# Kernel tuning notes

Hardware: AMD Instinct MI355X
Metric: run time of the kernel (lower is better)

The kernel has to match this reference:

```python
import jax, jax.numpy as jnp
import numpy as np

NB_HEAD = 8
SIZE_PER_HEAD = 64
MAX_LEN = 1024
MASK_PENALTY = 1e12


def setup_inputs() -> dict:
    key = jax.random.key(0)
    ks = jax.random.split(key, 6)
    B, L, D_IN = 8, MAX_LEN, 512
    D_OUT = NB_HEAD * SIZE_PER_HEAD
    return {
        "Q_seq": jax.random.normal(ks[0], (B, L, D_IN), dtype=jnp.float32),
        "K_seq": jax.random.normal(ks[1], (B, L, D_IN), dtype=jnp.float32),
        "V_seq": jax.random.normal(ks[2], (B, L, D_IN), dtype=jnp.float32),
        "WQ": jax.random.normal(ks[3], (D_IN, D_OUT), dtype=jnp.float32) * 0.03,
        "WK": jax.random.normal(ks[4], (D_IN, D_OUT), dtype=jnp.float32) * 0.03,
        "WV": jax.random.normal(ks[5], (D_IN, D_OUT), dtype=jnp.float32) * 0.03,
    }


def reference(Q_seq, K_seq, V_seq, WQ, WK, WV):
    B, L, _ = Q_seq.shape
    H, D = NB_HEAD, SIZE_PER_HEAD
    # project and split heads: [B, L, H*D] -> [B, H, L, D]
    q = (Q_seq @ WQ).reshape(B, L, H, D).transpose(0, 2, 1, 3)
    k = (K_seq @ WK).reshape(B, L, H, D).transpose(0, 2, 1, 3)
    v = (V_seq @ WV).reshape(B, L, H, D).transpose(0, 2, 1, 3)
    scale = 1.0 / jnp.sqrt(jnp.asarray(D, dtype=q.dtype))
    scores = jnp.einsum('bhqd,bhkd->bhqk', q, k) * scale  # [B,H,L,L]
    # Mask(): eye+cumsum construction == causal mask (penalize key > query)
    causal = jnp.triu(jnp.ones((L, L), dtype=scores.dtype), k=1)
    scores = scores - causal * MASK_PENALTY
    A = jax.nn.softmax(scores, axis=-1)
    O = jnp.einsum('bhqk,bhkd->bhqd', A, v)  # [B,H,L,D]
    return O.transpose(0, 2, 1, 3).reshape(B, L, H * D)
```

## Files before the change

kernel.cpp:

```cpp
#include <hip/hip_runtime.h>

#define NH 8
#define DH 64
#define SL 1024
#define NB 8
#define DIN 512
#define DOUT 512
#define PS 72

typedef __bf16 bf16x8 __attribute__((ext_vector_type(8)));
typedef float floatx4 __attribute__((ext_vector_type(4)));
typedef unsigned short ushortx8 __attribute__((ext_vector_type(8)));

__device__ __forceinline__ unsigned short f2bf(float f) {
    unsigned int u = __builtin_bit_cast(unsigned int, f);
    u += 0x7FFFu + ((u >> 16) & 1u);
    return (unsigned short)(u >> 16);
}

__device__ __forceinline__ floatx4 mfma_bf16(bf16x8 a, bf16x8 b, floatx4 c) {
    return __builtin_amdgcn_mfma_f32_16x16x32_bf16(a, b, c, 0, 0, 0);
}

__device__ __forceinline__ void gld_lds16(const unsigned short* g, unsigned short* l) {
    __builtin_amdgcn_global_load_lds(
        (const __attribute__((address_space(1))) unsigned int*)g,
        (__attribute__((address_space(3))) unsigned int*)l, 16, 0, 0);
}

__device__ __forceinline__ unsigned int pack_bf2(float a, float b) {
    return __builtin_amdgcn_perm(__builtin_bit_cast(unsigned int, b),
                                 __builtin_bit_cast(unsigned int, a), 0x07060302u);
}

__global__ __launch_bounds__(256) void xbf_kernel(const float* __restrict__ Qs,
                                                  const float* __restrict__ Ks,
                                                  const float* __restrict__ Vs,
                                                  unsigned short* __restrict__ xb) {
    const int z = blockIdx.y;
    const float* X = (z == 0) ? Qs : (z == 1 ? Ks : Vs);
    const int t = blockIdx.x * 256 + threadIdx.x;
    const int row = t >> 6, c = t & 63;
    const float4 a = *(const float4*)(X + t * 8);
    const float4 b = *(const float4*)(X + t * 8 + 4);
    ushortx8 o;
    o[0] = f2bf(a.x); o[1] = f2bf(a.y); o[2] = f2bf(a.z); o[3] = f2bf(a.w);
    o[4] = f2bf(b.x); o[5] = f2bf(b.y); o[6] = f2bf(b.z); o[7] = f2bf(b.w);
    const int dst = (((row >> 7) * 8 + (c >> 3)) * 128 + (row & 127)) * 64 +
                    (((c & 7) ^ (row & 7)) * 8);
    *(ushortx8*)(xb + z * 8192 * DIN + dst) = o;
}

__global__ __launch_bounds__(256) void wt_kernel(const float* __restrict__ WQ,
                                                 const float* __restrict__ WK,
                                                 const float* __restrict__ WV,
                                                 unsigned short* __restrict__ wt) {
    __shared__ unsigned short tile[64][68];
    const int z = blockIdx.z;
    const float* W = (z == 0) ? WQ : (z == 1 ? WK : WV);
    const int k0 = blockIdx.y * 64, n0 = blockIdx.x * 64;
    const int tn = threadIdx.x & 63, tk = threadIdx.x >> 6;
#pragma unroll
    for (int i = 0; i < 16; ++i) {
        const int kk = tk + i * 4;
        tile[tn][kk] = f2bf(W[(k0 + kk) * DOUT + n0 + tn]);
    }
    __syncthreads();
#pragma unroll
    for (int i = 0; i < 16; ++i) {
        const int nn = tk + i * 4;
        const int n = n0 + nn, k = k0 + tn;
        const int dst = (((z * 4 + (n >> 7)) * 8 + (k >> 6)) * 128 + (n & 127)) * 64 +
                        ((((k >> 3) & 7) ^ (n & 7)) * 8) + (k & 7);
        wt[dst] = tile[nn][tn];
    }
}

__global__ __launch_bounds__(256) void proj_kernel(const unsigned short* __restrict__ xbt,
                                                   const unsigned short* __restrict__ wtt,
                                                   unsigned short* __restrict__ qw,
                                                   unsigned short* __restrict__ ks,
                                                   unsigned short* __restrict__ vs) {
    __shared__ __align__(16) unsigned short S[16384];
    unsigned short* As = S;
    unsigned short* Bs = S + 8192;
    const int z = blockIdx.z;
    const int mblk = blockIdx.x, nblk = blockIdx.y;
    const int w = threadIdx.x >> 6, lane = threadIdx.x & 63;
    const int l15 = lane & 15, quad = lane >> 4;
    const int wm = w >> 1, wn = w & 1;
    const int soff = lane * 8;
    const unsigned short* Ab = xbt + z * (8192 * DIN) + mblk * 8 * 8192 + (w * 4) * 512 + soff;
    const unsigned short* Bb = wtt + (z * 4 + nblk) * 8 * 8192 + (w * 4) * 512 + soff;
    unsigned short* Asw = &As[(w * 4) * 512];
    unsigned short* Bsw = &Bs[(w * 4) * 512];

    floatx4 acc[4][4];
#pragma unroll
    for (int i = 0; i < 4; ++i)
#pragma unroll
        for (int j = 0; j < 4; ++j) acc[i][j] = floatx4{0.f, 0.f, 0.f, 0.f};

    for (int kblk = 0; kblk < 8; ++kblk) {
        __syncthreads();
#pragma unroll
        for (int i = 0; i < 4; ++i) {
            gld_lds16(Ab + kblk * 8192 + i * 512, Asw + i * 512);
            gld_lds16(Bb + kblk * 8192 + i * 512, Bsw + i * 512);
        }
        __syncthreads();
#pragma unroll
        for (int ksub = 0; ksub < 2; ++ksub) {
            bf16x8 af[4], bfr[4];
#pragma unroll
            for (int mi = 0; mi < 4; ++mi) {
                const int row = wm * 64 + mi * 16 + l15;
                af[mi] = *(const bf16x8*)&As[row * 64 + (((quad + ksub * 4) ^ (l15 & 7)) * 8)];
            }
#pragma unroll
            for (int nt = 0; nt < 4; ++nt) {
                const int row = wn * 64 + nt * 16 + l15;
                bfr[nt] = *(const bf16x8*)&Bs[row * 64 + (((quad + ksub * 4) ^ (l15 & 7)) * 8)];
            }
#pragma unroll
            for (int mi = 0; mi < 4; ++mi)
#pragma unroll
                for (int nt = 0; nt < 4; ++nt)
                    acc[mi][nt] = mfma_bf16(af[mi], bfr[nt], acc[mi][nt]);
        }
    }

    __syncthreads();
#pragma unroll
    for (int mi = 0; mi < 4; ++mi)
#pragma unroll
        for (int nt = 0; nt < 4; ++nt)
#pragma unroll
            for (int r = 0; r < 4; ++r) {
                const int a = wm * 64 + mi * 16 + quad * 4 + r;
                const int c = wn * 64 + nt * 16 + l15;
                const int h = c >> 6, dh = c & 63;
                float v = acc[mi][nt][r];
                int lidx;
                if (z == 0) {
                    v *= 0.18033688f;
                    lidx = h * 8192 + (a >> 4) * 1024 + (dh >> 3) * 128 + (a & 15) * 8 + (dh & 7);
                } else if (z == 1) {
                    lidx = (((((h << 3) + (a >> 4)) << 1) | (dh >> 5))) * 512 +
                           (a & 15) * 32 + (dh & 31);
                } else {
                    const int s64 = ((a & 15) << 2) | ((a >> 4) & 3);
                    lidx = ((((h << 1) | (a >> 6)) << 1) | (s64 >> 5)) * 2048 +
                           dh * 32 + (s64 & 31);
                }
                S[lidx] = f2bf(v);
            }
    __syncthreads();

    const int b = mblk >> 3;
    const int li0 = (mblk & 7) * 128;
    const int tid = threadIdx.x;
    unsigned short* outp = (z == 0) ? qw : (z == 1 ? ks : vs);
#pragma unroll
    for (int j = 0; j < 8; ++j) {
        const int off = j * 2048 + tid * 8;
        const ushortx8 val = *(const ushortx8*)(S + off);
        int gidx;
        if (z == 0) {
            const int h = off >> 13, o13 = off & 8191;
            gidx = ((b * 8 + nblk * 2 + h) * 64 + (li0 >> 4) + (o13 >> 10)) * 1024 + (o13 & 1023);
        } else if (z == 1) {
            const int region = off >> 9, pos = off & 511;
            const int h = region >> 4, g = (region >> 1) & 7, d5 = region & 1;
            gidx = (((b * 8 + nblk * 2 + h) * 64 + (li0 >> 4) + g) * 2 + d5) * 512 + pos;
        } else {
            const int region = off >> 11, pos = off & 2047;
            const int h = region >> 2, l6 = (region >> 1) & 1, s5 = region & 1;
            gidx = ((b * 8 + nblk * 2 + h) * 32 + (li0 >> 5) + l6 * 2 + s5) * 2048 + pos;
        }
        *(ushortx8*)(outp + gidx) = val;
    }
}

__global__ __launch_bounds__(256) void attn_kernel(const unsigned short* __restrict__ qw,
                                                   const unsigned short* __restrict__ ksp,
                                                   const unsigned short* __restrict__ vsp,
                                                   float* __restrict__ out) {
    __shared__ union {
        unsigned short Ps[4][16 * PS];
        float Cb[2][64][21];
    } sh;
    const int w = threadIdx.x >> 6;
    const int lane = threadIdx.x & 63;
    const int l15 = lane & 15, quad = lane >> 4;
    const int bh = blockIdx.y;
    const int b = bh >> 3, h = bh & 7;
    const int tile = (w < 2) ? blockIdx.x : 63 - blockIdx.x;
    const int half = w & 1;
    const int m0 = tile * 16;

    const unsigned short* qp = qw + (bh * 64 + tile) * 1024 + quad * 128 + l15 * 8;
    const bf16x8 aQ0 = *(const bf16x8*)qp;
    const bf16x8 aQ1 = *(const bf16x8*)(qp + 512);

    const unsigned short* ksb = ksp + (bh * 64) * 2 * 512 + l15 * 32 + quad * 8;
    const unsigned short* vsb = vsp + (bh * 32 * 64 + l15) * 32 + quad * 8;
    unsigned short* myPs = sh.Ps[w];

    float lrow[4] = {0.f, 0.f, 0.f, 0.f};
    floatx4 o0 = {0.f, 0.f, 0.f, 0.f}, o1 = o0, o2 = o0, o3 = o0;
    const floatx4 zf = {0.f, 0.f, 0.f, 0.f};

    auto TAIL = [&](int kt, floatx4* s, bool domask, const bf16x8* v0, const bf16x8* v1) {
#pragma unroll
        for (int r = 0; r < 4; ++r) {
            const int row = m0 + quad * 4 + r;
            float p[4];
#pragma unroll
            for (int t = 0; t < 4; ++t) {
                float e = __builtin_amdgcn_exp2f(s[t][r]);
                if (domask && (kt + t * 16 + l15 > row)) e = 0.f;
                p[t] = e;
            }
            lrow[r] += (p[0] + p[1]) + (p[2] + p[3]);
            uint2 pk;
            pk.x = pack_bf2(p[0], p[1]);
            pk.y = pack_bf2(p[2], p[3]);
            *(uint2*)(myPs + (quad * 4 + r) * PS + l15 * 4) = pk;
        }
        __builtin_amdgcn_wave_barrier();
        const bf16x8 aP0 = *(const bf16x8*)(myPs + l15 * PS + quad * 8);
        const bf16x8 aP1 = *(const bf16x8*)(myPs + l15 * PS + 32 + quad * 8);
        __builtin_amdgcn_wave_barrier();
        o0 = mfma_bf16(aP1, v1[0], mfma_bf16(aP0, v0[0], o0));
        o1 = mfma_bf16(aP1, v1[1], mfma_bf16(aP0, v0[1], o1));
        o2 = mfma_bf16(aP1, v1[2], mfma_bf16(aP0, v0[2], o2));
        o3 = mfma_bf16(aP1, v1[3], mfma_bf16(aP0, v0[3], o3));
    };

    auto BODY = [&](int kt) {
        const unsigned short* vb = vsb + (kt >> 5) * 2048;
        bf16x8 v0[4], v1[4];
#pragma unroll
        for (int dt = 0; dt < 4; ++dt) {
            v0[dt] = *(const bf16x8*)(vb + dt * 512);
            v1[dt] = *(const bf16x8*)(vb + dt * 512 + 2048);
        }
        const unsigned short* kp = ksb + (kt >> 4) * 1024;
        floatx4 s[4];
#pragma unroll
        for (int t = 0; t < 4; ++t) {
            const bf16x8 k0 = *(const bf16x8*)(kp + t * 1024);
            const bf16x8 k1 = *(const bf16x8*)(kp + t * 1024 + 512);
            s[t] = mfma_bf16(aQ1, k1, mfma_bf16(aQ0, k0, zf));
        }
        TAIL(kt, s, false, v0, v1);
    };

    auto BODYM = [&](int kt) {
        const unsigned short* vb = vsb + (kt >> 5) * 2048;
        bf16x8 v0[4], v1[4];
#pragma unroll
        for (int dt = 0; dt < 4; ++dt) {
            v0[dt] = *(const bf16x8*)(vb + dt * 512);
            v1[dt] = *(const bf16x8*)(vb + dt * 512 + 2048);
        }
        const unsigned short* kp = ksb + (kt >> 4) * 1024;
        floatx4 s[4] = {zf, zf, zf, zf};
#pragma unroll
        for (int t = 0; t < 4; ++t) {
            if (kt + t * 16 <= m0 + 15) {
                const bf16x8 k0 = *(const bf16x8*)(kp + t * 1024);
                const bf16x8 k1 = *(const bf16x8*)(kp + t * 1024 + 512);
                s[t] = mfma_bf16(aQ1, k1, mfma_bf16(aQ0, k0, zf));
            }
        }
        TAIL(kt, s, true, v0, v1);
    };

    const int nf = (tile + 4) >> 2;
    const int last = nf - 1;
    for (int j = half; j < last; j += 2) BODY(j * 64);
    if ((last & 1) == half) BODYM(last * 64);

    __syncthreads();
    if (half == 1) {
        float* cb = &sh.Cb[w >> 1][lane][0];
#pragma unroll
        for (int r = 0; r < 4; ++r) {
            cb[r] = o0[r]; cb[4 + r] = o1[r];
            cb[8 + r] = o2[r]; cb[12 + r] = o3[r];
            cb[16 + r] = lrow[r];
        }
    }
    __syncthreads();
    if (half == 0) {
        const float* cb = &sh.Cb[w >> 1][lane][0];
#pragma unroll
        for (int r = 0; r < 4; ++r) {
            o0[r] += cb[r]; o1[r] += cb[4 + r];
            o2[r] += cb[8 + r]; o3[r] += cb[12 + r];
            lrow[r] += cb[16 + r];
        }
#pragma unroll
        for (int r = 0; r < 4; ++r) {
            float l = lrow[r];
            l += __shfl_xor(l, 1);
            l += __shfl_xor(l, 2);
            l += __shfl_xor(l, 4);
            l += __shfl_xor(l, 8);
            const float inv = 1.0f / l;
            const int row = m0 + quad * 4 + r;
            float* op = out + (b * SL + row) * DOUT + h * DH + l15;
            op[0]  = o0[r] * inv;
            op[16] = o1[r] * inv;
            op[32] = o2[r] * inv;
            op[48] = o3[r] * inv;
        }
    }
}

extern "C" void kernel_launch(void* const* d_in, const int* in_sizes, int n_in,
                              void* d_out, int out_size, void* d_ws, size_t ws_size,
                              hipStream_t stream) {
    const float* Qs = (const float*)d_in[0];
    const float* Ks = (const float*)d_in[1];
    const float* Vs = (const float*)d_in[2];
    const float* WQ = (const float*)d_in[3];
    const float* WK = (const float*)d_in[4];
    const float* WV = (const float*)d_in[5];
    float* out = (float*)d_out;

    unsigned short* xb = (unsigned short*)d_ws;
    unsigned short* wt = xb + 3 * 8192 * DIN;
    unsigned short* qw = wt + 3 * DIN * DOUT;
    unsigned short* ks = qw + NB * NH * SL * DH;
    unsigned short* vs = ks + NB * NH * SL * DH;

    xbf_kernel<<<dim3(8192 * DIN / (256 * 8), 3), 256, 0, stream>>>(Qs, Ks, Vs, xb);
    wt_kernel<<<dim3(DOUT / 64, DIN / 64, 3), 256, 0, stream>>>(WQ, WK, WV, wt);
    proj_kernel<<<dim3(64, 4, 3), 256, 0, stream>>>(xb, wt, qw, ks, vs);
    attn_kernel<<<dim3(32, NB * NH), 256, 0, stream>>>(qw, ks, vs, out);
}
```

Baseline: 167.6 us.

## Merge prep kernels, remap projection blocks, raise MFMA wave priority

Fuses the activation bf16 conversion and the weight transpose into one prep kernel, which removes a launch and its tail. Remaps the projection grid so that consecutive workgroups are spread across m-blocks with the n-block in the low bits, changing cache reuse and distribution across XCDs. Wraps the MFMA sections of the attention loop in s_setprio so matrix work is issued ahead of the exp/pack phases of other waves. Each is a small independent scheduling tweak; the remapping may also change L2 locality.

```diff
diff --git a/kernel.cpp b/kernel.cpp
--- a/kernel.cpp
+++ b/kernel.cpp
@@ -33,46 +33,50 @@
                                  __builtin_bit_cast(unsigned int, a), 0x07060302u);
 }
 
-__global__ __launch_bounds__(256) void xbf_kernel(const float* __restrict__ Qs,
-                                                  const float* __restrict__ Ks,
-                                                  const float* __restrict__ Vs,
-                                                  unsigned short* __restrict__ xb) {
-    const int z = blockIdx.y;
-    const float* X = (z == 0) ? Qs : (z == 1 ? Ks : Vs);
-    const int t = blockIdx.x * 256 + threadIdx.x;
-    const int row = t >> 6, c = t & 63;
-    const float4 a = *(const float4*)(X + t * 8);
-    const float4 b = *(const float4*)(X + t * 8 + 4);
-    ushortx8 o;
-    o[0] = f2bf(a.x); o[1] = f2bf(a.y); o[2] = f2bf(a.z); o[3] = f2bf(a.w);
-    o[4] = f2bf(b.x); o[5] = f2bf(b.y); o[6] = f2bf(b.z); o[7] = f2bf(b.w);
-    const int dst = (((row >> 7) * 8 + (c >> 3)) * 128 + (row & 127)) * 64 +
-                    (((c & 7) ^ (row & 7)) * 8);
-    *(ushortx8*)(xb + z * 8192 * DIN + dst) = o;
-}
-
-__global__ __launch_bounds__(256) void wt_kernel(const float* __restrict__ WQ,
-                                                 const float* __restrict__ WK,
-                                                 const float* __restrict__ WV,
-                                                 unsigned short* __restrict__ wt) {
+__global__ __launch_bounds__(256) void prep_kernel(const float* __restrict__ Qs,
+                                                   const float* __restrict__ Ks,
+                                                   const float* __restrict__ Vs,
+                                                   const float* __restrict__ WQ,
+                                                   const float* __restrict__ WK,
+                                                   const float* __restrict__ WV,
+                                                   unsigned short* __restrict__ xb,
+                                                   unsigned short* __restrict__ wt) {
     __shared__ unsigned short tile[64][68];
-    const int z = blockIdx.z;
-    const float* W = (z == 0) ? WQ : (z == 1 ? WK : WV);
-    const int k0 = blockIdx.y * 64, n0 = blockIdx.x * 64;
-    const int tn = threadIdx.x & 63, tk = threadIdx.x >> 6;
-#pragma unroll
-    for (int i = 0; i < 16; ++i) {
-        const int kk = tk + i * 4;
-        tile[tn][kk] = f2bf(W[(k0 + kk) * DOUT + n0 + tn]);
-    }
-    __syncthreads();
-#pragma unroll
-    for (int i = 0; i < 16; ++i) {
-        const int nn = tk + i * 4;
-        const int n = n0 + nn, k = k0 + tn;
-        const int dst = (((z * 4 + (n >> 7)) * 8 + (k >> 6)) * 128 + (n & 127)) * 64 +
-                        ((((k >> 3) & 7) ^ (n & 7)) * 8) + (k & 7);
-        wt[dst] = tile[nn][tn];
+    const int bid = blockIdx.x;
+    if (bid < 6144) {
+        const int z = bid >> 11;
+        const float* X = (z == 0) ? Qs : (z == 1 ? Ks : Vs);
+        const int t = (bid & 2047) * 256 + threadIdx.x;
+        const int row = t >> 6, c = t & 63;
+        const float4 a = *(const float4*)(X + t * 8);
+        const float4 b = *(const float4*)(X + t * 8 + 4);
+        ushortx8 o;
+        o[0] = f2bf(a.x); o[1] = f2bf(a.y); o[2] = f2bf(a.z); o[3] = f2bf(a.w);
+        o[4] = f2bf(b.x); o[5] = f2bf(b.y); o[6] = f2bf(b.z); o[7] = f2bf(b.w);
+        const int dst = (((row >> 7) * 8 + (c >> 3)) * 128 + (row & 127)) * 64 +
+                        (((c & 7) ^ (row & 7)) * 8);
+        *(ushortx8*)(xb + z * 8192 * DIN + dst) = o;
+    } else {
+        const int b2 = bid - 6144;
+        const int z = b2 >> 6;
+        const int r = b2 & 63;
+        const float* W = (z == 0) ? WQ : (z == 1 ? WK : WV);
+        const int k0 = (r >> 3) * 64, n0 = (r & 7) * 64;
+        const int tn = threadIdx.x & 63, tk = threadIdx.x >> 6;
+#pragma unroll
+        for (int i = 0; i < 16; ++i) {
+            const int kk = tk + i * 4;
+            tile[tn][kk] = f2bf(W[(k0 + kk) * DOUT + n0 + tn]);
+        }
+        __syncthreads();
+#pragma unroll
+        for (int i = 0; i < 16; ++i) {
+            const int nn = tk + i * 4;
+            const int n = n0 + nn, k = k0 + tn;
+            const int dst = (((z * 4 + (n >> 7)) * 8 + (k >> 6)) * 128 + (n & 127)) * 64 +
+                            ((((k >> 3) & 7) ^ (n & 7)) * 8) + (k & 7);
+            wt[dst] = tile[nn][tn];
+        }
     }
 }
 
@@ -84,8 +88,11 @@
     __shared__ __align__(16) unsigned short S[16384];
     unsigned short* As = S;
     unsigned short* Bs = S + 8192;
-    const int z = blockIdx.z;
-    const int mblk = blockIdx.x, nblk = blockIdx.y;
+    const int z = blockIdx.y;
+    const int wg = blockIdx.x;
+    const int ix = wg >> 3;
+    const int mblk = (wg & 7) * 8 + (ix >> 2);
+    const int nblk = ix & 3;
     const int w = threadIdx.x >> 6, lane = threadIdx.x & 63;
     const int l15 = lane & 15, quad = lane >> 4;
     const int wm = w >> 1, wn = w & 1;
@@ -232,10 +239,12 @@
         const bf16x8 aP0 = *(const bf16x8*)(myPs + l15 * PS + quad * 8);
         const bf16x8 aP1 = *(const bf16x8*)(myPs + l15 * PS + 32 + quad * 8);
         __builtin_amdgcn_wave_barrier();
+        __builtin_amdgcn_s_setprio(1);
         o0 = mfma_bf16(aP1, v1[0], mfma_bf16(aP0, v0[0], o0));
         o1 = mfma_bf16(aP1, v1[1], mfma_bf16(aP0, v0[1], o1));
         o2 = mfma_bf16(aP1, v1[2], mfma_bf16(aP0, v0[2], o2));
         o3 = mfma_bf16(aP1, v1[3], mfma_bf16(aP0, v0[3], o3));
+        __builtin_amdgcn_s_setprio(0);
     };
 
     auto BODY = [&](int kt) {
@@ -248,12 +257,14 @@
         }
         const unsigned short* kp = ksb + (kt >> 4) * 1024;
         floatx4 s[4];
+        __builtin_amdgcn_s_setprio(1);
 #pragma unroll
         for (int t = 0; t < 4; ++t) {
             const bf16x8 k0 = *(const bf16x8*)(kp + t * 1024);
             const bf16x8 k1 = *(const bf16x8*)(kp + t * 1024 + 512);
             s[t] = mfma_bf16(aQ1, k1, mfma_bf16(aQ0, k0, zf));
         }
+        __builtin_amdgcn_s_setprio(0);
         TAIL(kt, s, false, v0, v1);
     };
 
@@ -267,6 +278,7 @@
         }
         const unsigned short* kp = ksb + (kt >> 4) * 1024;
         floatx4 s[4] = {zf, zf, zf, zf};
+        __builtin_amdgcn_s_setprio(1);
 #pragma unroll
         for (int t = 0; t < 4; ++t) {
             if (kt + t * 16 <= m0 + 15) {
@@ -275,6 +287,7 @@
                 s[t] = mfma_bf16(aQ1, k1, mfma_bf16(aQ0, k0, zf));
             }
         }
+        __builtin_amdgcn_s_setprio(0);
         TAIL(kt, s, true, v0, v1);
     };
 
@@ -337,8 +350,7 @@
     unsigned short* ks = qw + NB * NH * SL * DH;
     unsigned short* vs = ks + NB * NH * SL * DH;
 
-    xbf_kernel<<<dim3(8192 * DIN / (256 * 8), 3), 256, 0, stream>>>(Qs, Ks, Vs, xb);
-    wt_kernel<<<dim3(DOUT / 64, DIN / 64, 3), 256, 0, stream>>>(WQ, WK, WV, wt);
-    proj_kernel<<<dim3(64, 4, 3), 256, 0, stream>>>(xb, wt, qw, ks, vs);
+    prep_kernel<<<dim3(6336), 256, 0, stream>>>(Qs, Ks, Vs, WQ, WK, WV, xb, wt);
+    proj_kernel<<<dim3(256, 3), 256, 0, stream>>>(xb, wt, qw, ks, vs);
     attn_kernel<<<dim3(32, NB * NH), 256, 0, stream>>>(qw, ks, vs, out);
 }
```

Result: no change. 168.5 us (+0.5%).
